# Optimization experiments

Hardware: AMD Instinct MI355X
Metric: run time of the kernel (lower is better)

Reference implementation:

```python
import jax, jax.numpy as jnp
import numpy as np

NUM_SLOTS = 8
DIM = 256
ITERS = 3
EPS_LN = 1e-5

def _ln(x, g, b):
    mu = jnp.mean(x, axis=-1, keepdims=True)
    var = jnp.var(x, axis=-1, keepdims=True)
    return (x - mu) * jax.lax.rsqrt(var + EPS_LN) * g + b

def setup_inputs() -> dict:
    key = jax.random.key(0)
    ks = jax.random.split(key, 16)
    d = DIM
    s = 1.0 / np.sqrt(d)
    inp = {
        'x': jax.random.normal(ks[0], (64, 4096, d), jnp.float32),
        'noise': jax.random.normal(ks[1], (64, NUM_SLOTS, d), jnp.float32),
        'slots_mu': jax.random.normal(ks[2], (1, 1, d), jnp.float32),
        'slots_logsigma': jnp.zeros((1, 1, d), jnp.float32),
        'Wq': jax.random.uniform(ks[3], (d, d), jnp.float32, -s, s),
        'Wk': jax.random.uniform(ks[4], (d, d), jnp.float32, -s, s),
        'Wv': jax.random.uniform(ks[5], (d, d), jnp.float32, -s, s),
        'W_ih': jax.random.uniform(ks[6], (3 * d, d), jnp.float32, -s, s),
        'W_hh': jax.random.uniform(ks[7], (3 * d, d), jnp.float32, -s, s),
        'b_ih': jax.random.uniform(ks[8], (3 * d,), jnp.float32, -s, s),
        'b_hh': jax.random.uniform(ks[9], (3 * d,), jnp.float32, -s, s),
        'W1': jax.random.uniform(ks[10], (d, d), jnp.float32, -s, s),
        'b1': jax.random.uniform(ks[11], (d,), jnp.float32, -s, s),
        'W2': jax.random.uniform(ks[12], (d, d), jnp.float32, -s, s),
        'b2': jax.random.uniform(ks[13], (d,), jnp.float32, -s, s),
        'g_in': jnp.ones((d,), jnp.float32), 'be_in': jnp.zeros((d,), jnp.float32),
        'g_sl': jnp.ones((d,), jnp.float32), 'be_sl': jnp.zeros((d,), jnp.float32),
        'g_ff': jnp.ones((d,), jnp.float32), 'be_ff': jnp.zeros((d,), jnp.float32),
    }
    return inp

def _gru(x, h, W_ih, W_hh, b_ih, b_hh):
    # torch.nn.GRUCell math; x,h: [M, d]
    gi = x @ W_ih.T + b_ih
    gh = h @ W_hh.T + b_hh
    i_r, i_z, i_n = jnp.split(gi, 3, axis=-1)
    h_r, h_z, h_n = jnp.split(gh, 3, axis=-1)
    r = jax.nn.sigmoid(i_r + h_r)
    z = jax.nn.sigmoid(i_z + h_z)
    n = jnp.tanh(i_n + r * h_n)
    return (1.0 - z) * n + z * h

def reference(x, noise, slots_mu, slots_logsigma, Wq, Wk, Wv, W_ih, W_hh, b_ih, b_hh,
              W1, b1, W2, b2, g_in, be_in, g_sl, be_sl, g_ff, be_ff):
    B, N, d = x.shape
    scale = d ** (-0.5)
    x = _ln(x, g_in, be_in)
    slots = slots_mu + noise * jnp.exp(slots_logsigma)  # [B, K, d]
    # k/v are loop-invariant; hoist (same math as original)
    k = jnp.einsum('bnd,ed->bne', x, Wk)
    v = jnp.einsum('bnd,ed->bne', x, Wv)
    for _ in range(ITERS):
        slots_prev = slots
        q = jnp.einsum('bkd,ed->bke', _ln(slots, g_sl, be_sl), Wq)
        attn = jax.nn.softmax(jnp.einsum('bkd,bnd->bkn', q, k) * scale, axis=-1) + 1e-8
        attn = attn / jnp.sum(attn, axis=-1, keepdims=True)
        updates = jnp.einsum('bkn,bnd->bkd', attn, v)
        slots = _gru(updates.reshape(-1, d), slots_prev.reshape(-1, d),
                     W_ih, W_hh, b_ih, b_hh).reshape(B, NUM_SLOTS, d)
        h = jax.nn.relu(jnp.einsum('bkd,ed->bke', _ln(slots, g_ff, be_ff), W1) + b1)
        slots = slots + jnp.einsum('bkd,ed->bke', h, W2) + b2
    return slots.reshape(B, NUM_SLOTS * d)
```

## Files before the change

### kernel.cpp

```cpp
#include <hip/hip_runtime.h>
#include <cstddef>

#define DIM 256
#define NSLOT 8
#define BATCH 64
#define NTOK 4096
#define SEGB 16
#define NPART SEGB
#define ITERS 3
#define EPS 1e-5f

typedef short bf16x8 __attribute__((ext_vector_type(8)));
typedef short bf16x4 __attribute__((ext_vector_type(4)));
typedef float f32x4  __attribute__((ext_vector_type(4)));

static __device__ __forceinline__ short f2bf(float f) {
    union { float f; unsigned u; } v; v.f = f;
    unsigned r = v.u + 0x7fffu + ((v.u >> 16) & 1u);
    return (short)(r >> 16);
}

enum : size_t {
    OFF_M     = 0,
    OFF_WIHT  = OFF_M    + 256 * 256,
    OFF_WHHT  = OFF_WIHT + 256 * 768,
    OFF_WVT   = OFF_WHHT + 256 * 768,
    OFF_W1T   = OFF_WVT  + 256 * 256,
    OFF_W2T   = OFF_W1T  + 256 * 256,
    OFF_SLOTS = OFF_W2T  + 256 * 256,
    OFF_SNEW  = OFF_SLOTS + BATCH * NSLOT * 256,
    OFF_QT    = OFF_SNEW  + BATCH * NSLOT * 256,
    OFF_H     = OFF_QT    + BATCH * NSLOT * 256,
    OFF_UPD   = OFF_H     + BATCH * NSLOT * 256,
    OFF_UPART = OFF_UPD   + BATCH * NSLOT * 256,
    OFF_LPART = OFF_UPART + (size_t)BATCH * NPART * NSLOT * 256,
    OFF_XLN   = OFF_LPART + BATCH * NPART * 16,
    WS_FLOATS = OFF_XLN   + (size_t)BATCH * NTOK * 128
};

__global__ __launch_bounds__(256) void k_transpose(const float* __restrict__ w_ih,
                                                   const float* __restrict__ w_hh,
                                                   const float* __restrict__ wv,
                                                   const float* __restrict__ w1,
                                                   const float* __restrict__ w2,
                                                   float* __restrict__ ws) {
    int z = blockIdx.z;
    const float* src;
    float* dst;
    int R;
    if (z == 0)      { src = w_ih; dst = ws + OFF_WIHT; R = 768; }
    else if (z == 1) { src = w_hh; dst = ws + OFF_WHHT; R = 768; }
    else if (z == 2) { src = wv;   dst = ws + OFF_WVT;  R = 256; }
    else if (z == 3) { src = w1;   dst = ws + OFF_W1T;  R = 256; }
    else             { src = w2;   dst = ws + OFF_W2T;  R = 256; }
    if ((int)blockIdx.x * 32 >= R) return;
    __shared__ float tile[32][33];
    int lx = threadIdx.x & 31, ly = threadIdx.x >> 5;
    int r0 = blockIdx.x * 32, c0 = blockIdx.y * 32;
#pragma unroll
    for (int p = 0; p < 4; ++p)
        tile[ly + p * 8][lx] = src[(size_t)(r0 + ly + p * 8) * 256 + c0 + lx];
    __syncthreads();
#pragma unroll
    for (int p = 0; p < 4; ++p)
        dst[(size_t)(c0 + ly + p * 8) * R + r0 + lx] = tile[lx][ly + p * 8];
}

__global__ __launch_bounds__(256) void k_m(const float* __restrict__ wq,
                                           const float* __restrict__ wk,
                                           float* __restrict__ ws) {
    int d = blockIdx.x, t = threadIdx.x;
    float acc = 0.f;
    for (int e = 0; e < 256; ++e)
        acc += wq[e * 256 + d] * wk[e * 256 + t];
    ws[OFF_M + d * 256 + t] = acc * 0.0625f;
}

__global__ __launch_bounds__(256) void k_init(const float* __restrict__ mu,
                                              const float* __restrict__ logsig,
                                              const float* __restrict__ noise,
                                              float* __restrict__ ws) {
    int i = blockIdx.x * 256 + threadIdx.x;
    int d = i & 255;
    ws[OFF_SLOTS + i] = mu[d] + noise[i] * __expf(logsig[d]);
}

__global__ __launch_bounds__(256) void k_qt(float* __restrict__ ws,
                                            const float* __restrict__ g_sl,
                                            const float* __restrict__ be_sl) {
    __shared__ float ln[2048];
    int chunk = blockIdx.x, b = blockIdx.y;
    int t = threadIdx.x, wave = t >> 6, lane = t & 63;
    const float* slots = ws + OFF_SLOTS + b * 2048;
    float4 gf = ((const float4*)g_sl)[lane];
    float4 bf = ((const float4*)be_sl)[lane];
#pragma unroll
    for (int rr = 0; rr < 2; ++rr) {
        int r = wave + rr * 4;
        float4 v = ((const float4*)(slots + r * 256))[lane];
        float s1 = v.x + v.y + v.z + v.w;
        float s2 = v.x * v.x + v.y * v.y + v.z * v.z + v.w * v.w;
#pragma unroll
        for (int m = 1; m < 64; m <<= 1) { s1 += __shfl_xor(s1, m); s2 += __shfl_xor(s2, m); }
        float mu = s1 * (1.f / 256.f);
        float rstd = rsqrtf(s2 * (1.f / 256.f) - mu * mu + EPS);
        float4 o;
        o.x = (v.x - mu) * rstd * gf.x + bf.x;
        o.y = (v.y - mu) * rstd * gf.y + bf.y;
        o.z = (v.z - mu) * rstd * gf.z + bf.z;
        o.w = (v.w - mu) * rstd * gf.w + bf.w;
        *((float4*)&ln[r * 256 + lane * 4]) = o;
    }
    __syncthreads();
    const float* M = ws + OFF_M;
    int k0 = t >> 6;
    int e = chunk * 64 + (t & 63);
    float a0 = 0.f, a1 = 0.f;
    for (int d = 0; d < 256; ++d) {
        float m = M[d * 256 + e];
        a0 += ln[k0 * 256 + d] * m;
        a1 += ln[(k0 + 4) * 256 + d] * m;
    }
    float* qt = ws + OFF_QT + b * 2048;
    qt[k0 * 256 + e] = a0;
    qt[(k0 + 4) * 256 + e] = a1;
}

template <bool P1>
__global__ __launch_bounds__(256) void k_attn_t(const float* __restrict__ x,
                                                const float* __restrict__ g_in,
                                                const float* __restrict__ be_in,
                                                float* __restrict__ ws) {
    int seg = blockIdx.x, b = blockIdx.y;
    int t = threadIdx.x;
    int w = t >> 6, lane = t & 63;
    int q = lane >> 4, s16 = lane & 15;

    __shared__ short qhi[8 * 264];
    __shared__ short xT[256 * 64];
    __shared__ short Etmp[16 * 72];
    __shared__ float lsum[4][8];

    const float* qtg = ws + OFF_QT + b * 2048;
    for (int idx = t; idx < 8 * 264; idx += 256) {
        int s = idx >> 8;
        s = idx / 264;
        int d = idx - s * 264;
        qhi[idx] = (d < 256) ? f2bf(qtg[s * 256 + d]) : (short)0;
    }
    __syncthreads();

    bf16x8 qf[8];
#pragma unroll
    for (int i = 0; i < 8; ++i) {
        if (s16 < 8) qf[i] = *(const bf16x8*)&qhi[s16 * 264 + i * 32 + q * 8];
        else         qf[i] = (bf16x8){0, 0, 0, 0, 0, 0, 0, 0};
    }

    f32x4 U[4];
#pragma unroll
    for (int c = 0; c < 4; ++c) U[c] = (f32x4){0.f, 0.f, 0.f, 0.f};
    float lacc = 0.f;

    short* xln = (short*)(ws + OFF_XLN);
    int mytok = seg * 256 + w * 16 + s16;
    int g0 = ((w * 16 + s16) >> 3);
    int t7 = s16 & 7;

    bf16x8 af[8];
    if (!P1) {
        const short* xr = xln + ((size_t)b * NTOK + mytok) * 256 + q * 8;
#pragma unroll
        for (int i = 0; i < 8; ++i) af[i] = *(const bf16x8*)&xr[i * 32];
    }

    for (int tt = 0; tt < 4; ++tt) {
        int tok = mytok + tt * 64;
        if (P1) {
            const float4* xp = (const float4*)(x + ((size_t)b * NTOK + tok) * 256 + q * 8);
            float4 xa[8], xb[8];
#pragma unroll
            for (int i = 0; i < 8; ++i) { xa[i] = xp[8 * i]; xb[i] = xp[8 * i + 1]; }
            float s1 = 0.f, s2 = 0.f;
#pragma unroll
            for (int i = 0; i < 8; ++i) {
                s1 += xa[i].x + xa[i].y + xa[i].z + xa[i].w + xb[i].x + xb[i].y + xb[i].z + xb[i].w;
                s2 += xa[i].x * xa[i].x + xa[i].y * xa[i].y + xa[i].z * xa[i].z + xa[i].w * xa[i].w
                    + xb[i].x * xb[i].x + xb[i].y * xb[i].y + xb[i].z * xb[i].z + xb[i].w * xb[i].w;
            }
            s1 += __shfl_xor(s1, 16); s2 += __shfl_xor(s2, 16);
            s1 += __shfl_xor(s1, 32); s2 += __shfl_xor(s2, 32);
            float mu = s1 * (1.f / 256.f);
            float rstd = rsqrtf(s2 * (1.f / 256.f) - mu * mu + EPS);
            short* xrow = xln + ((size_t)b * NTOK + tok) * 256;
#pragma unroll
            for (int i = 0; i < 8; ++i) {
                int dbase = i * 32 + q * 8;
                float4 gA = *(const float4*)&g_in[dbase];
                float4 gB = *(const float4*)&g_in[dbase + 4];
                float4 bA = *(const float4*)&be_in[dbase];
                float4 bB = *(const float4*)&be_in[dbase + 4];
                bf16x8 f;
                f[0] = f2bf((xa[i].x - mu) * rstd * gA.x + bA.x);
                f[1] = f2bf((xa[i].y - mu) * rstd * gA.y + bA.y);
                f[2] = f2bf((xa[i].z - mu) * rstd * gA.z + bA.z);
                f[3] = f2bf((xa[i].w - mu) * rstd * gA.w + bA.w);
                f[4] = f2bf((xb[i].x - mu) * rstd * gB.x + bB.x);
                f[5] = f2bf((xb[i].y - mu) * rstd * gB.y + bB.y);
                f[6] = f2bf((xb[i].z - mu) * rstd * gB.z + bB.z);
                f[7] = f2bf((xb[i].w - mu) * rstd * gB.w + bB.w);
                af[i] = f;
                *(bf16x8*)&xrow[i * 32 + q * 8] = f;
            }
        }

        f32x4 Lc0 = (f32x4){0.f, 0.f, 0.f, 0.f};
        f32x4 Lc1 = (f32x4){0.f, 0.f, 0.f, 0.f};
#pragma unroll
        for (int i = 0; i < 4; ++i) {
            Lc0 = __builtin_amdgcn_mfma_f32_16x16x32_bf16(af[i],     qf[i],     Lc0, 0, 0, 0);
            Lc1 = __builtin_amdgcn_mfma_f32_16x16x32_bf16(af[i + 4], qf[i + 4], Lc1, 0, 0, 0);
        }

        bf16x4 e2;
#pragma unroll
        for (int r = 0; r < 4; ++r) {
            float E = __expf(fminf(Lc0[r] + Lc1[r], 30.f));
            lacc += E;
            e2[r] = f2bf(E);
        }

        __syncthreads();

#pragma unroll
        for (int i = 0; i < 8; ++i) {
            int Ki = (4 * i + q) & 7;
            int dbase = i * 32 + q * 8;
            bf16x8 f = af[i];
#pragma unroll
            for (int e = 0; e < 8; ++e) {
                int gp = (g0 ^ e ^ Ki) & 7;
                xT[((dbase + e) << 6) + (gp << 3) + t7] = f[e];
            }
        }
        *(bf16x4*)&Etmp[s16 * 72 + w * 16 + q * 4] = e2;

        __syncthreads();

        bf16x8 afn[8];
        if (!P1 && tt < 3) {
            const short* xr = xln + ((size_t)b * NTOK + tok + 64) * 256 + q * 8;
#pragma unroll
            for (int i = 0; i < 8; ++i) afn[i] = *(const bf16x8*)&xr[i * 32];
        }

        bf16x8 ea0 = *(const bf16x8*)&Etmp[s16 * 72 + q * 8];
        bf16x8 ea1 = *(const bf16x8*)&Etmp[s16 * 72 + 32 + q * 8];
#pragma unroll
        for (int c = 0; c < 4; ++c) {
            int d = (4 * w + c) * 16 + s16;
            int swz = (d ^ (d >> 3)) & 7;
            const short* row = &xT[d << 6];
            bf16x8 b0 = *(const bf16x8*)&row[((q ^ swz) & 7) << 3];
            bf16x8 b1 = *(const bf16x8*)&row[(((4 + q) ^ swz) & 7) << 3];
            U[c] = __builtin_amdgcn_mfma_f32_16x16x32_bf16(ea0, b0, U[c], 0, 0, 0);
            U[c] = __builtin_amdgcn_mfma_f32_16x16x32_bf16(ea1, b1, U[c], 0, 0, 0);
        }

        if (!P1 && tt < 3) {
#pragma unroll
            for (int i = 0; i < 8; ++i) af[i] = afn[i];
        }
    }

    lacc += __shfl_xor(lacc, 16); lacc += __shfl_xor(lacc, 32);
    __syncthreads();
    if (q == 0 && s16 < 8) lsum[w][s16] = lacc;
    __syncthreads();
    float* lpart = ws + OFF_LPART + (size_t)(b * NPART + seg) * 16;
    if (t < 8) lpart[t] = lsum[0][t] + lsum[1][t] + lsum[2][t] + lsum[3][t];
    float* up = ws + OFF_UPART + (size_t)(b * NPART + seg) * NSLOT * 256;
#pragma unroll
    for (int c = 0; c < 4; ++c) {
        int d = (4 * w + c) * 16 + s16;
#pragma unroll
        for (int r = 0; r < 4; ++r) {
            int slot = q * 4 + r;
            if (slot < 8) up[slot * 256 + d] = U[c][r];
        }
    }
}

static __device__ __forceinline__ void ln_row2(const float* src, float* dst,
                                               const float* __restrict__ g,
                                               const float* __restrict__ be,
                                               int wave, int lane) {
    if (wave < 2) {
        float4 v = *(const float4*)(src + wave * 256 + lane * 4);
        float s1 = v.x + v.y + v.z + v.w;
        float s2 = v.x * v.x + v.y * v.y + v.z * v.z + v.w * v.w;
#pragma unroll
        for (int m = 1; m < 64; m <<= 1) { s1 += __shfl_xor(s1, m); s2 += __shfl_xor(s2, m); }
        float mu = s1 * (1.f / 256.f);
        float rstd = rsqrtf(s2 * (1.f / 256.f) - mu * mu + EPS);
        float4 gf = ((const float4*)g)[lane];
        float4 bf = ((const float4*)be)[lane];
        float4 o;
        o.x = (v.x - mu) * rstd * gf.x + bf.x;
        o.y = (v.y - mu) * rstd * gf.y + bf.y;
        o.z = (v.z - mu) * rstd * gf.z + bf.z;
        o.w = (v.w - mu) * rstd * gf.w + bf.w;
        *(float4*)(dst + wave * 256 + lane * 4) = o;
    }
}

__global__ __launch_bounds__(512) void k_fused(float* __restrict__ ws,
                                               const float* __restrict__ b_ih,
                                               const float* __restrict__ b_hh,
                                               const float* __restrict__ g_ff,
                                               const float* __restrict__ be_ff,
                                               const float* __restrict__ b1p,
                                               const float* __restrict__ b2p,
                                               const float* __restrict__ g_sl,
                                               const float* __restrict__ be_sl,
                                               float* __restrict__ dout) {
    __shared__ __align__(16) float uc[2][256], upd[2][256], sl[2][256], snew[2][256];
    __shared__ __align__(16) float lnb[2][256], hbuf[2][256], so[2][256];
    __shared__ float lsv[2];

    int sp = blockIdx.x, b = blockIdx.y, t = threadIdx.x;
    int s0 = sp * 2;
    int s = t >> 8, d = t & 255;
    int wave = t >> 6, lane = t & 63;

    if (t < 32) {
        int ss = t >> 4, g = t & 15;
        float lv = ws[OFF_LPART + (size_t)(b * NPART + g) * 16 + s0 + ss];
#pragma unroll
        for (int m = 1; m < 16; m <<= 1) lv += __shfl_xor(lv, m);
        if ((t & 15) == 0) lsv[ss] = lv;
    }

    const float* up0 = ws + OFF_UPART + (size_t)b * NPART * NSLOT * 256 + (s0 + s) * 256 + d;
    float acc = 0.f;
#pragma unroll
    for (int g = 0; g < NPART; ++g) acc += up0[(size_t)g * NSLOT * 256];
    sl[s][d] = ws[OFF_SLOTS + (size_t)b * 2048 + (s0 + s) * 256 + d];
    __syncthreads();
    uc[s][d] = acc / lsv[s];
    __syncthreads();

    {
        const float* WvT = ws + OFF_WVT;
        float o = 0.f;
        for (int dd = 0; dd < 256; ++dd) o += uc[s][dd] * WvT[dd * 256 + d];
        upd[s][d] = o;
    }
    __syncthreads();

    {
        const float* WihT = ws + OFF_WIHT;
        const float* WhhT = ws + OFF_WHHT;
        float ar = 0.f, az = 0.f, an = 0.f, hr = 0.f, hz = 0.f, hn = 0.f;
        for (int dd = 0; dd < 256; ++dd) {
            float ud = upd[s][dd], sd = sl[s][dd];
            const float* wi = WihT + dd * 768;
            const float* wh = WhhT + dd * 768;
            ar += ud * wi[d];       az += ud * wi[256 + d]; an += ud * wi[512 + d];
            hr += sd * wh[d];       hz += sd * wh[256 + d]; hn += sd * wh[512 + d];
        }
        float rg = 1.f / (1.f + __expf(-(ar + b_ih[d] + hr + b_hh[d])));
        float zg = 1.f / (1.f + __expf(-(az + b_ih[256 + d] + hz + b_hh[256 + d])));
        float ng = tanhf(an + b_ih[512 + d] + rg * (hn + b_hh[512 + d]));
        snew[s][d] = (1.f - zg) * ng + zg * sl[s][d];
    }
    __syncthreads();

    ln_row2(&snew[0][0], &lnb[0][0], g_ff, be_ff, wave, lane);
    __syncthreads();

    {
        const float* W1T = ws + OFF_W1T;
        float o = 0.f;
        for (int dd = 0; dd < 256; ++dd) o += lnb[s][dd] * W1T[dd * 256 + d];
        hbuf[s][d] = fmaxf(o + b1p[d], 0.f);
    }
    __syncthreads();

    {
        const float* W2T = ws + OFF_W2T;
        float o = 0.f;
        for (int dd = 0; dd < 256; ++dd) o += hbuf[s][dd] * W2T[dd * 256 + d];
        float r = snew[s][d] + o + b2p[d];
        so[s][d] = r;
        ws[OFF_SLOTS + (size_t)b * 2048 + (s0 + s) * 256 + d] = r;
        if (dout) dout[(size_t)b * 2048 + (s0 + s) * 256 + d] = r;
    }

    if (!dout) {
        __syncthreads();
        ln_row2(&so[0][0], &lnb[0][0], g_sl, be_sl, wave, lane);
        __syncthreads();
        const float* M = ws + OFF_M;
        float o = 0.f;
        for (int dd = 0; dd < 256; ++dd) o += lnb[s][dd] * M[dd * 256 + d];
        ws[OFF_QT + (size_t)b * 2048 + (s0 + s) * 256 + d] = o;
    }
}

extern "C" void kernel_launch(void* const* d_in, const int* in_sizes, int n_in,
                              void* d_out, int out_size, void* d_ws, size_t ws_size,
                              hipStream_t stream) {
    const float* x      = (const float*)d_in[0];
    const float* noise  = (const float*)d_in[1];
    const float* mu     = (const float*)d_in[2];
    const float* logsig = (const float*)d_in[3];
    const float* Wq     = (const float*)d_in[4];
    const float* Wk     = (const float*)d_in[5];
    const float* Wv     = (const float*)d_in[6];
    const float* W_ih   = (const float*)d_in[7];
    const float* W_hh   = (const float*)d_in[8];
    const float* b_ih   = (const float*)d_in[9];
    const float* b_hh   = (const float*)d_in[10];
    const float* W1     = (const float*)d_in[11];
    const float* b1     = (const float*)d_in[12];
    const float* W2     = (const float*)d_in[13];
    const float* b2     = (const float*)d_in[14];
    const float* g_in   = (const float*)d_in[15];
    const float* be_in  = (const float*)d_in[16];
    const float* g_sl   = (const float*)d_in[17];
    const float* be_sl  = (const float*)d_in[18];
    const float* g_ff   = (const float*)d_in[19];
    const float* be_ff  = (const float*)d_in[20];
    float* ws = (float*)d_ws;
    float* out = (float*)d_out;

    hipLaunchKernelGGL(k_transpose, dim3(24, 8, 5), dim3(256), 0, stream, W_ih, W_hh, Wv, W1, W2, ws);
    hipLaunchKernelGGL(k_m, dim3(256), dim3(256), 0, stream, Wq, Wk, ws);
    hipLaunchKernelGGL(k_init, dim3(512), dim3(256), 0, stream, mu, logsig, noise, ws);
    hipLaunchKernelGGL(k_qt, dim3(4, 64), dim3(256), 0, stream, ws, g_sl, be_sl);
    for (int it = 0; it < ITERS; ++it) {
        if (it == 0)
            hipLaunchKernelGGL((k_attn_t<true>),  dim3(SEGB, 64), dim3(256), 0, stream, x, g_in, be_in, ws);
        else
            hipLaunchKernelGGL((k_attn_t<false>), dim3(SEGB, 64), dim3(256), 0, stream, x, g_in, be_in, ws);
        hipLaunchKernelGGL(k_fused, dim3(4, 64), dim3(512), 0, stream, ws,
                           b_ih, b_hh, g_ff, be_ff, b1, b2, g_sl, be_sl,
                           (it == ITERS - 1) ? out : nullptr);
    }
}
```

Before: 732.0 us.

## Fuse slot update into attention kernel via last-block atomic counter

Merges the three setup kernels into one launch and folds the per-batch GRU/MLP slot update into the attention kernel. The last-finishing segment block for each batch is detected with an atomic counter and does the reduction and update. That block now handles all 8 slots with 256 threads, so each weight load is reused across 8 slots. This removes several kernel launches and the separate k_fused pass. The cost is that the tail work per batch is serialized onto a single block, which may leave most CUs idle during that phase.

```diff
diff --git a/kernel.cpp b/kernel.cpp
--- a/kernel.cpp
+++ b/kernel.cpp
@@ -38,51 +38,63 @@
     WS_FLOATS = OFF_XLN   + (size_t)BATCH * NTOK * 128
 };
 
-__global__ __launch_bounds__(256) void k_transpose(const float* __restrict__ w_ih,
-                                                   const float* __restrict__ w_hh,
-                                                   const float* __restrict__ wv,
-                                                   const float* __restrict__ w1,
-                                                   const float* __restrict__ w2,
-                                                   float* __restrict__ ws) {
-    int z = blockIdx.z;
-    const float* src;
-    float* dst;
-    int R;
-    if (z == 0)      { src = w_ih; dst = ws + OFF_WIHT; R = 768; }
-    else if (z == 1) { src = w_hh; dst = ws + OFF_WHHT; R = 768; }
-    else if (z == 2) { src = wv;   dst = ws + OFF_WVT;  R = 256; }
-    else if (z == 3) { src = w1;   dst = ws + OFF_W1T;  R = 256; }
-    else             { src = w2;   dst = ws + OFF_W2T;  R = 256; }
-    if ((int)blockIdx.x * 32 >= R) return;
-    __shared__ float tile[32][33];
-    int lx = threadIdx.x & 31, ly = threadIdx.x >> 5;
-    int r0 = blockIdx.x * 32, c0 = blockIdx.y * 32;
-#pragma unroll
-    for (int p = 0; p < 4; ++p)
-        tile[ly + p * 8][lx] = src[(size_t)(r0 + ly + p * 8) * 256 + c0 + lx];
-    __syncthreads();
-#pragma unroll
-    for (int p = 0; p < 4; ++p)
-        dst[(size_t)(c0 + ly + p * 8) * R + r0 + lx] = tile[lx][ly + p * 8];
-}
-
-__global__ __launch_bounds__(256) void k_m(const float* __restrict__ wq,
-                                           const float* __restrict__ wk,
-                                           float* __restrict__ ws) {
-    int d = blockIdx.x, t = threadIdx.x;
-    float acc = 0.f;
-    for (int e = 0; e < 256; ++e)
-        acc += wq[e * 256 + d] * wk[e * 256 + t];
-    ws[OFF_M + d * 256 + t] = acc * 0.0625f;
-}
-
-__global__ __launch_bounds__(256) void k_init(const float* __restrict__ mu,
-                                              const float* __restrict__ logsig,
-                                              const float* __restrict__ noise,
-                                              float* __restrict__ ws) {
-    int i = blockIdx.x * 256 + threadIdx.x;
-    int d = i & 255;
-    ws[OFF_SLOTS + i] = mu[d] + noise[i] * __expf(logsig[d]);
+union MegaShared {
+    struct {
+        short qhi[8 * 264];
+        short xT[256 * 64];
+        short Etmp[16 * 72];
+        float lsum[4][8];
+    } a;
+    struct {
+        float uc[8][256];
+        float sl[8][256];
+        float t1[8][256];
+        float lsum8[8];
+    } tl;
+};
+
+__global__ __launch_bounds__(256) void k_pre(const float* __restrict__ w_ih,
+                                             const float* __restrict__ w_hh,
+                                             const float* __restrict__ wv,
+                                             const float* __restrict__ w1,
+                                             const float* __restrict__ w2,
+                                             const float* __restrict__ wq,
+                                             const float* __restrict__ wk,
+                                             const float* __restrict__ mu,
+                                             const float* __restrict__ logsig,
+                                             const float* __restrict__ noise,
+                                             float* __restrict__ ws) {
+    int u = blockIdx.x, t = threadIdx.x;
+    if (u < 576) {
+        const float* src; float* dst; int R, idx;
+        if (u < 192)      { src = w_ih; dst = ws + OFF_WIHT; R = 768; idx = u; }
+        else if (u < 384) { src = w_hh; dst = ws + OFF_WHHT; R = 768; idx = u - 192; }
+        else if (u < 448) { src = wv;   dst = ws + OFF_WVT;  R = 256; idx = u - 384; }
+        else if (u < 512) { src = w1;   dst = ws + OFF_W1T;  R = 256; idx = u - 448; }
+        else              { src = w2;   dst = ws + OFF_W2T;  R = 256; idx = u - 512; }
+        int bx = idx >> 3, by = idx & 7;
+        __shared__ float tile[32][33];
+        int lx = t & 31, ly = t >> 5;
+        int r0 = bx * 32, c0 = by * 32;
+#pragma unroll
+        for (int p = 0; p < 4; ++p)
+            tile[ly + p * 8][lx] = src[(size_t)(r0 + ly + p * 8) * 256 + c0 + lx];
+        __syncthreads();
+#pragma unroll
+        for (int p = 0; p < 4; ++p)
+            dst[(size_t)(c0 + ly + p * 8) * R + r0 + lx] = tile[lx][ly + p * 8];
+    } else if (u < 832) {
+        int d = u - 576;
+        if (d == 0 && t < 192) ((int*)(ws + OFF_UPD))[t] = 0;
+        float acc = 0.f;
+        for (int e = 0; e < 256; ++e)
+            acc += wq[e * 256 + d] * wk[e * 256 + t];
+        ws[OFF_M + d * 256 + t] = acc * 0.0625f;
+    } else {
+        int i = (u - 832) * 256 + t;
+        int d = i & 255;
+        ws[OFF_SLOTS + i] = mu[d] + noise[i] * __expf(logsig[d]);
+    }
 }
 
 __global__ __launch_bounds__(256) void k_qt(float* __restrict__ ws,
@@ -126,34 +138,63 @@
     qt[(k0 + 4) * 256 + e] = a1;
 }
 
-template <bool P1>
-__global__ __launch_bounds__(256) void k_attn_t(const float* __restrict__ x,
-                                                const float* __restrict__ g_in,
-                                                const float* __restrict__ be_in,
-                                                float* __restrict__ ws) {
+static __device__ __forceinline__ void ln8(const float (*__restrict__ src)[256],
+                                           float (*__restrict__ dst)[256],
+                                           const float* __restrict__ g,
+                                           const float* __restrict__ be, int t) {
+    int wv = t >> 6, lane = t & 63;
+    float4 gf = ((const float4*)g)[lane];
+    float4 bf = ((const float4*)be)[lane];
+#pragma unroll
+    for (int rr = 0; rr < 2; ++rr) {
+        int r = wv + rr * 4;
+        float4 v = *(const float4*)&src[r][lane * 4];
+        float s1 = v.x + v.y + v.z + v.w;
+        float s2 = v.x * v.x + v.y * v.y + v.z * v.z + v.w * v.w;
+#pragma unroll
+        for (int m = 1; m < 64; m <<= 1) { s1 += __shfl_xor(s1, m); s2 += __shfl_xor(s2, m); }
+        float mu = s1 * (1.f / 256.f);
+        float rstd = rsqrtf(s2 * (1.f / 256.f) - mu * mu + EPS);
+        float4 o;
+        o.x = (v.x - mu) * rstd * gf.x + bf.x;
+        o.y = (v.y - mu) * rstd * gf.y + bf.y;
+        o.z = (v.z - mu) * rstd * gf.z + bf.z;
+        o.w = (v.w - mu) * rstd * gf.w + bf.w;
+        *(float4*)&dst[r][lane * 4] = o;
+    }
+}
+
+template <int IT>
+__global__ __launch_bounds__(256) void k_attn_it(
+        const float* __restrict__ x,
+        const float* __restrict__ g_in, const float* __restrict__ be_in,
+        const float* __restrict__ b_ih, const float* __restrict__ b_hh,
+        const float* __restrict__ g_ff, const float* __restrict__ be_ff,
+        const float* __restrict__ b1p, const float* __restrict__ b2p,
+        const float* __restrict__ g_sl, const float* __restrict__ be_sl,
+        float* __restrict__ ws, float* __restrict__ dout) {
+    constexpr bool p1 = (IT == 0);
+    constexpr bool last = (IT == ITERS - 1);
+    __shared__ MegaShared sh;
+    __shared__ int lastflag;
+
     int seg = blockIdx.x, b = blockIdx.y;
     int t = threadIdx.x;
     int w = t >> 6, lane = t & 63;
     int q = lane >> 4, s16 = lane & 15;
 
-    __shared__ short qhi[8 * 264];
-    __shared__ short xT[256 * 64];
-    __shared__ short Etmp[16 * 72];
-    __shared__ float lsum[4][8];
-
     const float* qtg = ws + OFF_QT + b * 2048;
     for (int idx = t; idx < 8 * 264; idx += 256) {
-        int s = idx >> 8;
-        s = idx / 264;
+        int s = idx / 264;
         int d = idx - s * 264;
-        qhi[idx] = (d < 256) ? f2bf(qtg[s * 256 + d]) : (short)0;
+        sh.a.qhi[idx] = (d < 256) ? f2bf(qtg[s * 256 + d]) : (short)0;
     }
     __syncthreads();
 
     bf16x8 qf[8];
 #pragma unroll
     for (int i = 0; i < 8; ++i) {
-        if (s16 < 8) qf[i] = *(const bf16x8*)&qhi[s16 * 264 + i * 32 + q * 8];
+        if (s16 < 8) qf[i] = *(const bf16x8*)&sh.a.qhi[s16 * 264 + i * 32 + q * 8];
         else         qf[i] = (bf16x8){0, 0, 0, 0, 0, 0, 0, 0};
     }
 
@@ -168,7 +209,7 @@
     int t7 = s16 & 7;
 
     bf16x8 af[8];
-    if (!P1) {
+    if (!p1) {
         const short* xr = xln + ((size_t)b * NTOK + mytok) * 256 + q * 8;
 #pragma unroll
         for (int i = 0; i < 8; ++i) af[i] = *(const bf16x8*)&xr[i * 32];
@@ -176,17 +217,15 @@
 
     for (int tt = 0; tt < 4; ++tt) {
         int tok = mytok + tt * 64;
-        if (P1) {
+        if (p1) {
             const float4* xp = (const float4*)(x + ((size_t)b * NTOK + tok) * 256 + q * 8);
-            float4 xa[8], xb[8];
-#pragma unroll
-            for (int i = 0; i < 8; ++i) { xa[i] = xp[8 * i]; xb[i] = xp[8 * i + 1]; }
             float s1 = 0.f, s2 = 0.f;
 #pragma unroll
             for (int i = 0; i < 8; ++i) {
-                s1 += xa[i].x + xa[i].y + xa[i].z + xa[i].w + xb[i].x + xb[i].y + xb[i].z + xb[i].w;
-                s2 += xa[i].x * xa[i].x + xa[i].y * xa[i].y + xa[i].z * xa[i].z + xa[i].w * xa[i].w
-                    + xb[i].x * xb[i].x + xb[i].y * xb[i].y + xb[i].z * xb[i].z + xb[i].w * xb[i].w;
+                float4 a = xp[8 * i], bv = xp[8 * i + 1];
+                s1 += a.x + a.y + a.z + a.w + bv.x + bv.y + bv.z + bv.w;
+                s2 += a.x * a.x + a.y * a.y + a.z * a.z + a.w * a.w
+                    + bv.x * bv.x + bv.y * bv.y + bv.z * bv.z + bv.w * bv.w;
             }
             s1 += __shfl_xor(s1, 16); s2 += __shfl_xor(s2, 16);
             s1 += __shfl_xor(s1, 32); s2 += __shfl_xor(s2, 32);
@@ -195,22 +234,23 @@
             short* xrow = xln + ((size_t)b * NTOK + tok) * 256;
 #pragma unroll
             for (int i = 0; i < 8; ++i) {
+                float4 a = xp[8 * i], bv = xp[8 * i + 1];
                 int dbase = i * 32 + q * 8;
                 float4 gA = *(const float4*)&g_in[dbase];
                 float4 gB = *(const float4*)&g_in[dbase + 4];
                 float4 bA = *(const float4*)&be_in[dbase];
                 float4 bB = *(const float4*)&be_in[dbase + 4];
                 bf16x8 f;
-                f[0] = f2bf((xa[i].x - mu) * rstd * gA.x + bA.x);
-                f[1] = f2bf((xa[i].y - mu) * rstd * gA.y + bA.y);
-                f[2] = f2bf((xa[i].z - mu) * rstd * gA.z + bA.z);
-                f[3] = f2bf((xa[i].w - mu) * rstd * gA.w + bA.w);
-                f[4] = f2bf((xb[i].x - mu) * rstd * gB.x + bB.x);
-                f[5] = f2bf((xb[i].y - mu) * rstd * gB.y + bB.y);
-                f[6] = f2bf((xb[i].z - mu) * rstd * gB.z + bB.z);
-                f[7] = f2bf((xb[i].w - mu) * rstd * gB.w + bB.w);
+                f[0] = f2bf((a.x - mu) * rstd * gA.x + bA.x);
+                f[1] = f2bf((a.y - mu) * rstd * gA.y + bA.y);
+                f[2] = f2bf((a.z - mu) * rstd * gA.z + bA.z);
+                f[3] = f2bf((a.w - mu) * rstd * gA.w + bA.w);
+                f[4] = f2bf((bv.x - mu) * rstd * gB.x + bB.x);
+                f[5] = f2bf((bv.y - mu) * rstd * gB.y + bB.y);
+                f[6] = f2bf((bv.z - mu) * rstd * gB.z + bB.z);
+                f[7] = f2bf((bv.w - mu) * rstd * gB.w + bB.w);
                 af[i] = f;
-                *(bf16x8*)&xrow[i * 32 + q * 8] = f;
+                *(bf16x8*)&xrow[dbase] = f;
             }
         }
 
@@ -240,45 +280,39 @@
 #pragma unroll
             for (int e = 0; e < 8; ++e) {
                 int gp = (g0 ^ e ^ Ki) & 7;
-                xT[((dbase + e) << 6) + (gp << 3) + t7] = f[e];
+                sh.a.xT[((dbase + e) << 6) + (gp << 3) + t7] = f[e];
             }
         }
-        *(bf16x4*)&Etmp[s16 * 72 + w * 16 + q * 4] = e2;
-
-        __syncthreads();
-
-        bf16x8 afn[8];
-        if (!P1 && tt < 3) {
+        *(bf16x4*)&sh.a.Etmp[s16 * 72 + w * 16 + q * 4] = e2;
+
+        __syncthreads();
+
+        if (!p1 && tt < 3) {
             const short* xr = xln + ((size_t)b * NTOK + tok + 64) * 256 + q * 8;
 #pragma unroll
-            for (int i = 0; i < 8; ++i) afn[i] = *(const bf16x8*)&xr[i * 32];
-        }
-
-        bf16x8 ea0 = *(const bf16x8*)&Etmp[s16 * 72 + q * 8];
-        bf16x8 ea1 = *(const bf16x8*)&Etmp[s16 * 72 + 32 + q * 8];
+            for (int i = 0; i < 8; ++i) af[i] = *(const bf16x8*)&xr[i * 32];
+        }
+
+        bf16x8 ea0 = *(const bf16x8*)&sh.a.Etmp[s16 * 72 + q * 8];
+        bf16x8 ea1 = *(const bf16x8*)&sh.a.Etmp[s16 * 72 + 32 + q * 8];
 #pragma unroll
         for (int c = 0; c < 4; ++c) {
             int d = (4 * w + c) * 16 + s16;
             int swz = (d ^ (d >> 3)) & 7;
-            const short* row = &xT[d << 6];
+            const short* row = &sh.a.xT[d << 6];
             bf16x8 b0 = *(const bf16x8*)&row[((q ^ swz) & 7) << 3];
             bf16x8 b1 = *(const bf16x8*)&row[(((4 + q) ^ swz) & 7) << 3];
             U[c] = __builtin_amdgcn_mfma_f32_16x16x32_bf16(ea0, b0, U[c], 0, 0, 0);
             U[c] = __builtin_amdgcn_mfma_f32_16x16x32_bf16(ea1, b1, U[c], 0, 0, 0);
         }
-
-        if (!P1 && tt < 3) {
-#pragma unroll
-            for (int i = 0; i < 8; ++i) af[i] = afn[i];
-        }
     }
 
     lacc += __shfl_xor(lacc, 16); lacc += __shfl_xor(lacc, 32);
     __syncthreads();
-    if (q == 0 && s16 < 8) lsum[w][s16] = lacc;
+    if (q == 0 && s16 < 8) sh.a.lsum[w][s16] = lacc;
     __syncthreads();
     float* lpart = ws + OFF_LPART + (size_t)(b * NPART + seg) * 16;
-    if (t < 8) lpart[t] = lsum[0][t] + lsum[1][t] + lsum[2][t] + lsum[3][t];
+    if (t < 8) lpart[t] = sh.a.lsum[0][t] + sh.a.lsum[1][t] + sh.a.lsum[2][t] + sh.a.lsum[3][t];
     float* up = ws + OFF_UPART + (size_t)(b * NPART + seg) * NSLOT * 256;
 #pragma unroll
     for (int c = 0; c < 4; ++c) {
@@ -289,122 +323,136 @@
             if (slot < 8) up[slot * 256 + d] = U[c][r];
         }
     }
-}
-
-static __device__ __forceinline__ void ln_row2(const float* src, float* dst,
-                                               const float* __restrict__ g,
-                                               const float* __restrict__ be,
-                                               int wave, int lane) {
-    if (wave < 2) {
-        float4 v = *(const float4*)(src + wave * 256 + lane * 4);
-        float s1 = v.x + v.y + v.z + v.w;
-        float s2 = v.x * v.x + v.y * v.y + v.z * v.z + v.w * v.w;
-#pragma unroll
-        for (int m = 1; m < 64; m <<= 1) { s1 += __shfl_xor(s1, m); s2 += __shfl_xor(s2, m); }
-        float mu = s1 * (1.f / 256.f);
-        float rstd = rsqrtf(s2 * (1.f / 256.f) - mu * mu + EPS);
-        float4 gf = ((const float4*)g)[lane];
-        float4 bf = ((const float4*)be)[lane];
-        float4 o;
-        o.x = (v.x - mu) * rstd * gf.x + bf.x;
-        o.y = (v.y - mu) * rstd * gf.y + bf.y;
-        o.z = (v.z - mu) * rstd * gf.z + bf.z;
-        o.w = (v.w - mu) * rstd * gf.w + bf.w;
-        *(float4*)(dst + wave * 256 + lane * 4) = o;
-    }
-}
-
-__global__ __launch_bounds__(512) void k_fused(float* __restrict__ ws,
-                                               const float* __restrict__ b_ih,
-                                               const float* __restrict__ b_hh,
-                                               const float* __restrict__ g_ff,
-                                               const float* __restrict__ be_ff,
-                                               const float* __restrict__ b1p,
-                                               const float* __restrict__ b2p,
-                                               const float* __restrict__ g_sl,
-                                               const float* __restrict__ be_sl,
-                                               float* __restrict__ dout) {
-    __shared__ __align__(16) float uc[2][256], upd[2][256], sl[2][256], snew[2][256];
-    __shared__ __align__(16) float lnb[2][256], hbuf[2][256], so[2][256];
-    __shared__ float lsv[2];
-
-    int sp = blockIdx.x, b = blockIdx.y, t = threadIdx.x;
-    int s0 = sp * 2;
-    int s = t >> 8, d = t & 255;
-    int wave = t >> 6, lane = t & 63;
-
-    if (t < 32) {
-        int ss = t >> 4, g = t & 15;
-        float lv = ws[OFF_LPART + (size_t)(b * NPART + g) * 16 + s0 + ss];
-#pragma unroll
-        for (int m = 1; m < 16; m <<= 1) lv += __shfl_xor(lv, m);
-        if ((t & 15) == 0) lsv[ss] = lv;
-    }
-
-    const float* up0 = ws + OFF_UPART + (size_t)b * NPART * NSLOT * 256 + (s0 + s) * 256 + d;
-    float acc = 0.f;
-#pragma unroll
-    for (int g = 0; g < NPART; ++g) acc += up0[(size_t)g * NSLOT * 256];
-    sl[s][d] = ws[OFF_SLOTS + (size_t)b * 2048 + (s0 + s) * 256 + d];
-    __syncthreads();
-    uc[s][d] = acc / lsv[s];
+
+    if (t == 0) lastflag = 0;
+    __threadfence();
+    __syncthreads();
+    int* cnt = (int*)(ws + OFF_UPD) + IT * 64 + b;
+    if (t == 0) {
+        if (atomicAdd(cnt, 1) == NPART - 1) lastflag = 1;
+    }
+    __syncthreads();
+    if (!lastflag) return;
+    __threadfence();
+    if (t == 0) *cnt = 0;
+
+    if (t < 8) {
+        float l = 0.f;
+        for (int g = 0; g < NPART; ++g)
+            l += ws[OFF_LPART + (size_t)(b * NPART + g) * 16 + t];
+        sh.tl.lsum8[t] = l;
+    }
+#pragma unroll
+    for (int s = 0; s < 8; ++s) {
+        float a = 0.f;
+        const float* base = ws + OFF_UPART + (size_t)b * (NPART * 2048) + s * 256 + t;
+        for (int g = 0; g < NPART; ++g) a += base[(size_t)g * 2048];
+        sh.tl.t1[s][t] = a;
+        sh.tl.sl[s][t] = ws[OFF_SLOTS + (size_t)b * 2048 + s * 256 + t];
+    }
+    __syncthreads();
+#pragma unroll
+    for (int s = 0; s < 8; ++s) sh.tl.uc[s][t] = sh.tl.t1[s][t] / sh.tl.lsum8[s];
     __syncthreads();
 
     {
-        const float* WvT = ws + OFF_WVT;
-        float o = 0.f;
-        for (int dd = 0; dd < 256; ++dd) o += uc[s][dd] * WvT[dd * 256 + d];
-        upd[s][d] = o;
+        const float* W = ws + OFF_WVT;
+        float acc[8] = {0.f, 0.f, 0.f, 0.f, 0.f, 0.f, 0.f, 0.f};
+        for (int dd = 0; dd < 256; ++dd) {
+            float wv = W[dd * 256 + t];
+#pragma unroll
+            for (int s = 0; s < 8; ++s) acc[s] += sh.tl.uc[s][dd] * wv;
+        }
+        __syncthreads();
+#pragma unroll
+        for (int s = 0; s < 8; ++s) sh.tl.t1[s][t] = acc[s];
     }
     __syncthreads();
 
     {
-        const float* WihT = ws + OFF_WIHT;
-        const float* WhhT = ws + OFF_WHHT;
-        float ar = 0.f, az = 0.f, an = 0.f, hr = 0.f, hz = 0.f, hn = 0.f;
+        const float* WI = ws + OFF_WIHT;
+        const float* WH = ws + OFF_WHHT;
+        float bi0 = b_ih[t], bi1 = b_ih[256 + t], bi2 = b_ih[512 + t];
+        float bh0 = b_hh[t], bh1 = b_hh[256 + t], bh2 = b_hh[512 + t];
+        for (int p = 0; p < 4; ++p) {
+            int sA = 2 * p, sB = 2 * p + 1;
+            float ar0 = 0.f, az0 = 0.f, an0 = 0.f, hr0 = 0.f, hz0 = 0.f, hn0 = 0.f;
+            float ar1 = 0.f, az1 = 0.f, an1 = 0.f, hr1 = 0.f, hz1 = 0.f, hn1 = 0.f;
+            for (int dd = 0; dd < 256; ++dd) {
+                const float* wi = WI + (size_t)dd * 768;
+                const float* wh = WH + (size_t)dd * 768;
+                float wi0 = wi[t], wi1 = wi[256 + t], wi2 = wi[512 + t];
+                float wh0 = wh[t], wh1 = wh[256 + t], wh2 = wh[512 + t];
+                float u0 = sh.tl.t1[sA][dd], u1 = sh.tl.t1[sB][dd];
+                float v0 = sh.tl.sl[sA][dd], v1 = sh.tl.sl[sB][dd];
+                ar0 += u0 * wi0; az0 += u0 * wi1; an0 += u0 * wi2;
+                hr0 += v0 * wh0; hz0 += v0 * wh1; hn0 += v0 * wh2;
+                ar1 += u1 * wi0; az1 += u1 * wi1; an1 += u1 * wi2;
+                hr1 += v1 * wh0; hz1 += v1 * wh1; hn1 += v1 * wh2;
+            }
+            float rg0 = 1.f / (1.f + __expf(-(ar0 + bi0 + hr0 + bh0)));
+            float zg0 = 1.f / (1.f + __expf(-(az0 + bi1 + hz0 + bh1)));
+            float ng0 = tanhf(an0 + bi2 + rg0 * (hn0 + bh2));
+            sh.tl.uc[sA][t] = (1.f - zg0) * ng0 + zg0 * sh.tl.sl[sA][t];
+            float rg1 = 1.f / (1.f + __expf(-(ar1 + bi0 + hr1 + bh0)));
+            float zg1 = 1.f / (1.f + __expf(-(az1 + bi1 + hz1 + bh1)));
+            float ng1 = tanhf(an1 + bi2 + rg1 * (hn1 + bh2));
+            sh.tl.uc[sB][t] = (1.f - zg1) * ng1 + zg1 * sh.tl.sl[sB][t];
+        }
+    }
+    __syncthreads();
+
+    ln8(sh.tl.uc, sh.tl.t1, g_ff, be_ff, t);
+    __syncthreads();
+
+    {
+        const float* W = ws + OFF_W1T;
+        float acc[8] = {0.f, 0.f, 0.f, 0.f, 0.f, 0.f, 0.f, 0.f};
         for (int dd = 0; dd < 256; ++dd) {
-            float ud = upd[s][dd], sd = sl[s][dd];
-            const float* wi = WihT + dd * 768;
-            const float* wh = WhhT + dd * 768;
-            ar += ud * wi[d];       az += ud * wi[256 + d]; an += ud * wi[512 + d];
-            hr += sd * wh[d];       hz += sd * wh[256 + d]; hn += sd * wh[512 + d];
-        }
-        float rg = 1.f / (1.f + __expf(-(ar + b_ih[d] + hr + b_hh[d])));
-        float zg = 1.f / (1.f + __expf(-(az + b_ih[256 + d] + hz + b_hh[256 + d])));
-        float ng = tanhf(an + b_ih[512 + d] + rg * (hn + b_hh[512 + d]));
-        snew[s][d] = (1.f - zg) * ng + zg * sl[s][d];
-    }
-    __syncthreads();
-
-    ln_row2(&snew[0][0], &lnb[0][0], g_ff, be_ff, wave, lane);
+            float wv = W[dd * 256 + t];
+#pragma unroll
+            for (int s = 0; s < 8; ++s) acc[s] += sh.tl.t1[s][dd] * wv;
+        }
+        __syncthreads();
+        float bb = b1p[t];
+#pragma unroll
+        for (int s = 0; s < 8; ++s) sh.tl.sl[s][t] = fmaxf(acc[s] + bb, 0.f);
+    }
     __syncthreads();
 
     {
-        const float* W1T = ws + OFF_W1T;
-        float o = 0.f;
-        for (int dd = 0; dd < 256; ++dd) o += lnb[s][dd] * W1T[dd * 256 + d];
-        hbuf[s][d] = fmaxf(o + b1p[d], 0.f);
-    }
-    __syncthreads();
-
-    {
-        const float* W2T = ws + OFF_W2T;
-        float o = 0.f;
-        for (int dd = 0; dd < 256; ++dd) o += hbuf[s][dd] * W2T[dd * 256 + d];
-        float r = snew[s][d] + o + b2p[d];
-        so[s][d] = r;
-        ws[OFF_SLOTS + (size_t)b * 2048 + (s0 + s) * 256 + d] = r;
-        if (dout) dout[(size_t)b * 2048 + (s0 + s) * 256 + d] = r;
-    }
-
-    if (!dout) {
-        __syncthreads();
-        ln_row2(&so[0][0], &lnb[0][0], g_sl, be_sl, wave, lane);
+        const float* W = ws + OFF_W2T;
+        float acc[8] = {0.f, 0.f, 0.f, 0.f, 0.f, 0.f, 0.f, 0.f};
+        for (int dd = 0; dd < 256; ++dd) {
+            float wv = W[dd * 256 + t];
+#pragma unroll
+            for (int s = 0; s < 8; ++s) acc[s] += sh.tl.sl[s][dd] * wv;
+        }
+        __syncthreads();
+        float bb = b2p[t];
+#pragma unroll
+        for (int s = 0; s < 8; ++s) {
+            float r = sh.tl.uc[s][t] + acc[s] + bb;
+            sh.tl.t1[s][t] = r;
+            ws[OFF_SLOTS + (size_t)b * 2048 + s * 256 + t] = r;
+            if (last) dout[(size_t)b * 2048 + s * 256 + t] = r;
+        }
+    }
+
+    if (!last) {
+        __syncthreads();
+        ln8(sh.tl.t1, sh.tl.uc, g_sl, be_sl, t);
         __syncthreads();
         const float* M = ws + OFF_M;
-        float o = 0.f;
-        for (int dd = 0; dd < 256; ++dd) o += lnb[s][dd] * M[dd * 256 + d];
-        ws[OFF_QT + (size_t)b * 2048 + (s0 + s) * 256 + d] = o;
+        float acc[8] = {0.f, 0.f, 0.f, 0.f, 0.f, 0.f, 0.f, 0.f};
+        for (int dd = 0; dd < 256; ++dd) {
+            float m = M[dd * 256 + t];
+#pragma unroll
+            for (int s = 0; s < 8; ++s) acc[s] += sh.tl.uc[s][dd] * m;
+        }
+#pragma unroll
+        for (int s = 0; s < 8; ++s)
+            ws[OFF_QT + (size_t)b * 2048 + s * 256 + t] = acc[s];
     }
 }
 
@@ -435,17 +483,14 @@
     float* ws = (float*)d_ws;
     float* out = (float*)d_out;
 
-    hipLaunchKernelGGL(k_transpose, dim3(24, 8, 5), dim3(256), 0, stream, W_ih, W_hh, Wv, W1, W2, ws);
-    hipLaunchKernelGGL(k_m, dim3(256), dim3(256), 0, stream, Wq, Wk, ws);
-    hipLaunchKernelGGL(k_init, dim3(512), dim3(256), 0, stream, mu, logsig, noise, ws);
+    hipLaunchKernelGGL(k_pre, dim3(1344), dim3(256), 0, stream,
+                       W_ih, W_hh, Wv, W1, W2, Wq, Wk, mu, logsig, noise, ws);
     hipLaunchKernelGGL(k_qt, dim3(4, 64), dim3(256), 0, stream, ws, g_sl, be_sl);
-    for (int it = 0; it < ITERS; ++it) {
-        if (it == 0)
-            hipLaunchKernelGGL((k_attn_t<true>),  dim3(SEGB, 64), dim3(256), 0, stream, x, g_in, be_in, ws);
-        else
-            hipLaunchKernelGGL((k_attn_t<false>), dim3(SEGB, 64), dim3(256), 0, stream, x, g_in, be_in, ws);
-        hipLaunchKernelGGL(k_fused, dim3(4, 64), dim3(512), 0, stream, ws,
-                           b_ih, b_hh, g_ff, be_ff, b1, b2, g_sl, be_sl,
-                           (it == ITERS - 1) ? out : nullptr);
-    }
-}
+
+    hipLaunchKernelGGL((k_attn_it<0>), dim3(SEGB, 64), dim3(256), 0, stream,
+                       x, g_in, be_in, b_ih, b_hh, g_ff, be_ff, b1, b2, g_sl, be_sl, ws, out);
+    hipLaunchKernelGGL((k_attn_it<1>), dim3(SEGB, 64), dim3(256), 0, stream,
+                       x, g_in, be_in, b_ih, b_hh, g_ff, be_ff, b1, b2, g_sl, be_sl, ws, out);
+    hipLaunchKernelGGL((k_attn_it<2>), dim3(SEGB, 64), dim3(256), 0, stream,
+                       x, g_in, be_in, b_ih, b_hh, g_ff, be_ff, b1, b2, g_sl, be_sl, ws, out);
+}
```

Result: slower. 2.094 ms (+186.1%).
